# Optimization experiments

Hardware: AMD Instinct MI355X
Metric: run time of the kernel (lower is better)

The kernel has to match this reference:

```python
import jax, jax.numpy as jnp
import numpy as np

N_QUBITS = 5
N_A = 1
Q_DEPTH = 6
PATCH = 2 ** (N_QUBITS - N_A)  # 16


def _cz_sign(w):
    # diagonal sign of CZ on wires (w, w+1) over a (2,)*N_QUBITS state grid
    s = np.ones((2,) * N_QUBITS, np.float32)
    idx = [slice(None)] * N_QUBITS
    idx[w] = 1
    idx[w + 1] = 1
    s[tuple(idx)] = -1.0
    return jnp.asarray(s)

CZ_SIGNS = [_cz_sign(w) for w in range(N_QUBITS - 1)]


def apply_ry(state, theta, wire):
    # state: (B, 2,2,2,2,2) real amplitudes; theta: scalar or (B,)
    c = jnp.cos(theta * 0.5)
    s = jnp.sin(theta * 0.5)
    if jnp.ndim(c) == 1:  # per-sample angle
        c = c[:, None, None, None, None]
        s = s[:, None, None, None, None]
    st = jnp.moveaxis(state, 1 + wire, -1)
    a0, a1 = st[..., 0], st[..., 1]
    out = jnp.stack([c * a0 - s * a1, s * a0 + c * a1], axis=-1)
    return jnp.moveaxis(out, -1, 1 + wire)


def run_generator(noise, weights):
    # noise: (B, 5) per-sample angles; weights: (6, 5) shared angles
    B = noise.shape[0]
    state = jnp.zeros((B,) + (2,) * N_QUBITS, noise.dtype)
    state = state.at[(slice(None),) + (0,) * N_QUBITS].set(1.0)  # |00000>
    for w in range(N_QUBITS):
        state = apply_ry(state, noise[:, w], w)
    for d in range(Q_DEPTH):
        for w in range(N_QUBITS):
            state = apply_ry(state, weights[d, w], w)
        for w in range(N_QUBITS - 1):
            state = state * CZ_SIGNS[w]
    # RY/CZ are real, so probs = amplitude^2; unitary => sum(probs)=1
    probs = state.reshape(B, 2 ** N_QUBITS) ** 2
    p0 = probs[:, :PATCH]
    p0 = p0 / jnp.sum(probs, axis=1, keepdims=True)
    return p0 / jnp.max(p0, axis=1, keepdims=True)


def setup_inputs() -> dict:
    key = jax.random.key(0)
    k1, k2 = jax.random.split(key)
    B, C, H, W = 262144, 1, 4, 4
    inp = jax.random.normal(k1, (B, C, H, W), dtype=jnp.float32)
    q_params = jax.random.uniform(k2, (4, Q_DEPTH * N_QUBITS), dtype=jnp.float32)  # q_delta=1
    return {"input": inp, "q_params": q_params}


def reference(input, q_params):
    B, C, H, W = input.shape
    k = 2  # scale_factor
    # bilinear (half-pixel / align_corners=False) upsample
    up = jax.image.resize(input, (B, C, H * k, W * k), method='linear')
    noise = up.reshape(B, -1)[:, :N_QUBITS]  # 5 angles per sample
    outs = [run_generator(noise, q_params[g].reshape(Q_DEPTH, N_QUBITS))
            for g in range(q_params.shape[0])]
    return jnp.concatenate(outs, axis=1)  # (B, n_generators * 16)
```

## Files before the change

kernel.cpp:

```cpp
#include <hip/hip_runtime.h>

#define NQ   5
#define QD   6
#define NGEN 4
#define NW   (NGEN * QD * NQ)

__global__ __launch_bounds__(128) void qsrgan_build(
    const float* __restrict__ qp,
    float* __restrict__ M)
{
    __shared__ float cw[NW];
    __shared__ float sw[NW];
    const int t = threadIdx.x;
    if (t < NW) {
        float sv, cv;
        __sincosf(0.5f * qp[t], &sv, &cv);
        cw[t] = cv;
        sw[t] = sv;
    }
    __syncthreads();

    const int g = t >> 5;
    const int basis = t & 31;

    float st[32];
#pragma unroll
    for (int i = 0; i < 32; ++i) st[i] = (i == basis) ? 1.0f : 0.0f;

    for (int d = 0; d < QD; ++d) {
        const int base = g * (QD * NQ) + d * NQ;
#pragma unroll
        for (int w = 0; w < NQ; ++w) {
            const float cc = cw[base + w];
            const float ss = sw[base + w];
            const int stride = 1 << (4 - w);
#pragma unroll
            for (int i = 0; i < 32; ++i) {
                if (i & stride) continue;
                float a0 = st[i];
                float a1 = st[i + stride];
                st[i]          = cc * a0 - ss * a1;
                st[i + stride] = ss * a0 + cc * a1;
            }
        }
#pragma unroll
        for (int i = 0; i < 32; ++i) {
            int flips = 0;
#pragma unroll
            for (int w = 0; w < NQ - 1; ++w) {
                const int m = (1 << (4 - w)) | (1 << (3 - w));
                flips ^= ((i & m) == m) ? 1 : 0;
            }
            if (flips) st[i] = -st[i];
        }
    }

#pragma unroll
    for (int j = 0; j < 16; ++j)
        M[g * 512 + j * 32 + basis] = st[j];
}

__global__ __launch_bounds__(256, 8) void qsrgan_apply(
    const float* __restrict__ inp,
    const float* __restrict__ M,
    float* __restrict__ out,
    int B)
{
    __shared__ float pl[64 * 66];

    const int t    = threadIdx.x;
    const int lane = t & 63;
    const int g    = __builtin_amdgcn_readfirstlane(t >> 6);
    const int s0   = blockIdx.x * 64;
    const int b    = min(s0 + lane, B - 1);

    const float4 x = *reinterpret_cast<const float4*>(inp + (size_t)b * 16);
    float n[5];
    n[0] = x.x;
    n[1] = 0.75f * x.x + 0.25f * x.y;
    n[2] = 0.25f * x.x + 0.75f * x.y;
    n[3] = 0.75f * x.y + 0.25f * x.z;
    n[4] = 0.25f * x.y + 0.75f * x.z;

    float cn[5], sn[5];
#pragma unroll
    for (int w = 0; w < 5; ++w) __sincosf(0.5f * n[w], &sn[w], &cn[w]);

    float a4[4], a8[8], a16[16], init[32];
    {
        float a2[2] = {cn[4], sn[4]};
#pragma unroll
        for (int i = 0; i < 4; ++i)  a4[i]  = ((i >> 1) ? sn[3] : cn[3]) * a2[i & 1];
#pragma unroll
        for (int i = 0; i < 8; ++i)  a8[i]  = ((i >> 2) ? sn[2] : cn[2]) * a4[i & 3];
#pragma unroll
        for (int i = 0; i < 16; ++i) a16[i] = ((i >> 3) ? sn[1] : cn[1]) * a8[i & 7];
#pragma unroll
        for (int i = 0; i < 32; ++i) init[i] = ((i >> 4) ? sn[0] : cn[0]) * a16[i & 15];
    }

    const float* __restrict__ Mg = M + g * 512;
    float p[16];
    float mx = 0.0f;
#pragma unroll
    for (int j = 0; j < 16; ++j) {
        float acc = 0.0f;
#pragma unroll
        for (int k = 0; k < 32; ++k)
            acc += Mg[j * 32 + k] * init[k];
        p[j] = acc * acc;
        mx = fmaxf(mx, p[j]);
    }
    const float inv = 1.0f / mx;

#pragma unroll
    for (int j = 0; j < 16; ++j)
        pl[(g * 16 + j) * 66 + lane] = p[j] * inv;

    __syncthreads();

    const size_t base = (size_t)s0 * 64;
    float4* __restrict__ o4 = reinterpret_cast<float4*>(out + base);
#pragma unroll
    for (int i = 0; i < 4; ++i) {
        const int q    = t + i * 256;
        const int srow = q >> 4;
        const int c0   = (q & 15) << 2;
        if (s0 + srow < B) {
            float4 v;
            v.x = pl[(c0 + 0) * 66 + srow];
            v.y = pl[(c0 + 1) * 66 + srow];
            v.z = pl[(c0 + 2) * 66 + srow];
            v.w = pl[(c0 + 3) * 66 + srow];
            o4[q] = v;
        }
    }
}

extern "C" void kernel_launch(void* const* d_in, const int* in_sizes, int n_in,
                              void* d_out, int out_size, void* d_ws, size_t ws_size,
                              hipStream_t stream) {
    const float* inp = (const float*)d_in[0];
    const float* qp  = (const float*)d_in[1];
    float* out = (float*)d_out;
    float* M   = (float*)d_ws;
    const int B = in_sizes[0] / 16;

    qsrgan_build<<<1, 128, 0, stream>>>(qp, M);
    const int blocks = (B + 63) / 64;
    qsrgan_apply<<<blocks, 256, 0, stream>>>(inp, M, out, B);
}
```

Baseline: 96.69 us.

## Move circuit-matrix apply onto bf16 MFMA with split hi/lo precision

```diff
diff --git a/kernel.cpp b/kernel.cpp
--- a/kernel.cpp
+++ b/kernel.cpp
@@ -5,9 +5,22 @@
 #define NGEN 4
 #define NW   (NGEN * QD * NQ)
 
+typedef float f32x4 __attribute__((ext_vector_type(4)));
+typedef short short8 __attribute__((ext_vector_type(8)));
+
+__device__ inline unsigned short f2bf_rne(float f) {
+    unsigned u = __float_as_uint(f);
+    u += 0x7FFFu + ((u >> 16) & 1u);
+    return (unsigned short)(u >> 16);
+}
+__device__ inline float bf2f(unsigned short h) {
+    return __uint_as_float(((unsigned)h) << 16);
+}
+
 __global__ __launch_bounds__(128) void qsrgan_build(
     const float* __restrict__ qp,
-    float* __restrict__ M)
+    unsigned short* __restrict__ Bh,
+    unsigned short* __restrict__ Bl)
 {
     __shared__ float cw[NW];
     __shared__ float sw[NW];
@@ -56,13 +69,21 @@
     }
 
 #pragma unroll
-    for (int j = 0; j < 16; ++j)
-        M[g * 512 + j * 32 + basis] = st[j];
+    for (int j = 0; j < 16; ++j) {
+        const float v = st[j];
+        const unsigned short hi = f2bf_rne(v);
+        const float r = v - bf2f(hi);
+        const unsigned short lo = f2bf_rne(r);
+        const int idx = ((g * 4 + (basis >> 3)) * 16 + j) * 8 + (basis & 7);
+        Bh[idx] = hi;
+        Bl[idx] = lo;
+    }
 }
 
-__global__ __launch_bounds__(256, 8) void qsrgan_apply(
+__global__ __launch_bounds__(256, 4) void qsrgan_apply(
     const float* __restrict__ inp,
-    const float* __restrict__ M,
+    const unsigned short* __restrict__ Bh,
+    const unsigned short* __restrict__ Bl,
     float* __restrict__ out,
     int B)
 {
@@ -70,52 +91,77 @@
 
     const int t    = threadIdx.x;
     const int lane = t & 63;
-    const int g    = __builtin_amdgcn_readfirstlane(t >> 6);
+    const int w    = t >> 6;
+    const int q    = lane >> 4;
+    const int c    = lane & 15;
     const int s0   = blockIdx.x * 64;
-    const int b    = min(s0 + lane, B - 1);
 
-    const float4 x = *reinterpret_cast<const float4*>(inp + (size_t)b * 16);
+    const int bsmp = min(s0 + w * 16 + c, B - 1);
+    const float4 x = *reinterpret_cast<const float4*>(inp + (size_t)bsmp * 16);
+
+    short8 bh[4], bl[4];
+    const short8* gh = reinterpret_cast<const short8*>(Bh);
+    const short8* gl = reinterpret_cast<const short8*>(Bl);
+#pragma unroll
+    for (int g = 0; g < 4; ++g) {
+        bh[g] = gh[g * 64 + lane];
+        bl[g] = gl[g * 64 + lane];
+    }
+
     float n[5];
     n[0] = x.x;
     n[1] = 0.75f * x.x + 0.25f * x.y;
     n[2] = 0.25f * x.x + 0.75f * x.y;
     n[3] = 0.75f * x.y + 0.25f * x.z;
     n[4] = 0.25f * x.y + 0.75f * x.z;
-
     float cn[5], sn[5];
 #pragma unroll
-    for (int w = 0; w < 5; ++w) __sincosf(0.5f * n[w], &sn[w], &cn[w]);
+    for (int i = 0; i < 5; ++i) {
+        sn[i] = __sinf(0.5f * n[i]);
+        cn[i] = __cosf(0.5f * n[i]);
+    }
+    const float U = ((q >> 1) ? sn[0] : cn[0]) * ((q & 1) ? sn[1] : cn[1]);
+    float w34[4];
+    w34[0] = cn[3] * cn[4];
+    w34[1] = cn[3] * sn[4];
+    w34[2] = sn[3] * cn[4];
+    w34[3] = sn[3] * sn[4];
 
-    float a4[4], a8[8], a16[16], init[32];
-    {
-        float a2[2] = {cn[4], sn[4]};
+    short8 ah, al;
 #pragma unroll
-        for (int i = 0; i < 4; ++i)  a4[i]  = ((i >> 1) ? sn[3] : cn[3]) * a2[i & 1];
-#pragma unroll
-        for (int i = 0; i < 8; ++i)  a8[i]  = ((i >> 2) ? sn[2] : cn[2]) * a4[i & 3];
-#pragma unroll
-        for (int i = 0; i < 16; ++i) a16[i] = ((i >> 3) ? sn[1] : cn[1]) * a8[i & 7];
-#pragma unroll
-        for (int i = 0; i < 32; ++i) init[i] = ((i >> 4) ? sn[0] : cn[0]) * a16[i & 15];
+    for (int j = 0; j < 8; ++j) {
+        const float a = U * ((j >> 2) ? sn[2] : cn[2]) * w34[j & 3];
+        const unsigned short hi = f2bf_rne(a);
+        const float r = a - bf2f(hi);
+        ah[j] = (short)hi;
+        al[j] = (short)f2bf_rne(r);
     }
 
-    const float* __restrict__ Mg = M + g * 512;
-    float p[16];
-    float mx = 0.0f;
+    f32x4 acc[4];
 #pragma unroll
-    for (int j = 0; j < 16; ++j) {
-        float acc = 0.0f;
-#pragma unroll
-        for (int k = 0; k < 32; ++k)
-            acc += Mg[j * 32 + k] * init[k];
-        p[j] = acc * acc;
-        mx = fmaxf(mx, p[j]);
+    for (int g = 0; g < 4; ++g) {
+        f32x4 a0 = {0.0f, 0.0f, 0.0f, 0.0f};
+        a0 = __builtin_amdgcn_mfma_f32_16x16x32_bf16(ah, bh[g], a0, 0, 0, 0);
+        a0 = __builtin_amdgcn_mfma_f32_16x16x32_bf16(al, bh[g], a0, 0, 0, 0);
+        a0 = __builtin_amdgcn_mfma_f32_16x16x32_bf16(ah, bl[g], a0, 0, 0, 0);
+        acc[g] = a0;
     }
-    const float inv = 1.0f / mx;
 
 #pragma unroll
-    for (int j = 0; j < 16; ++j)
-        pl[(g * 16 + j) * 66 + lane] = p[j] * inv;
+    for (int g = 0; g < 4; ++g) {
+#pragma unroll
+        for (int r = 0; r < 4; ++r) {
+            const float d = acc[g][r];
+            float p = d * d;
+            float m = p;
+            m = fmaxf(m, __shfl_xor(m, 1));
+            m = fmaxf(m, __shfl_xor(m, 2));
+            m = fmaxf(m, __shfl_xor(m, 4));
+            m = fmaxf(m, __shfl_xor(m, 8));
+            const float v = p * (1.0f / m);
+            pl[(g * 16 + c) * 66 + (w * 16 + q * 4 + r)] = v;
+        }
+    }
 
     __syncthreads();
 
@@ -123,16 +169,16 @@
     float4* __restrict__ o4 = reinterpret_cast<float4*>(out + base);
 #pragma unroll
     for (int i = 0; i < 4; ++i) {
-        const int q    = t + i * 256;
-        const int srow = q >> 4;
-        const int c0   = (q & 15) << 2;
+        const int qq   = t + i * 256;
+        const int srow = qq >> 4;
+        const int c0   = (qq & 15) << 2;
         if (s0 + srow < B) {
             float4 v;
             v.x = pl[(c0 + 0) * 66 + srow];
             v.y = pl[(c0 + 1) * 66 + srow];
             v.z = pl[(c0 + 2) * 66 + srow];
             v.w = pl[(c0 + 3) * 66 + srow];
-            o4[q] = v;
+            o4[qq] = v;
         }
     }
 }
@@ -143,10 +189,11 @@
     const float* inp = (const float*)d_in[0];
     const float* qp  = (const float*)d_in[1];
     float* out = (float*)d_out;
-    float* M   = (float*)d_ws;
+    unsigned short* Bh = (unsigned short*)d_ws;
+    unsigned short* Bl = (unsigned short*)d_ws + 2048;
     const int B = in_sizes[0] / 16;
 
-    qsrgan_build<<<1, 128, 0, stream>>>(qp, M);
+    qsrgan_build<<<1, 128, 0, stream>>>(qp, Bh, Bl);
     const int blocks = (B + 63) / 64;
-    qsrgan_apply<<<blocks, 256, 0, stream>>>(inp, M, out, B);
+    qsrgan_apply<<<blocks, 256, 0, stream>>>(inp, Bh, Bl, out, B);
 }
```

Result: no change. 97.01 us (+0.3%).
